# Kernel optimization log

Measured on AMD Instinct MI355X. Metric: run time of the kernel, lower is better.

The kernel has to match this reference:

```python
import jax, jax.numpy as jnp
import numpy as np
from jax import lax

B, C, L, O, H, W = 256, 768, 64, 768, 9, 9
C2, C3 = 2 * C // 3, C // 3  # convh_2 / convl_1 output channels


def _c1x1(x, w, b):
    # 1x1 conv, w: (out,in), x: (b,in,h,w)
    return jnp.einsum('oc,bchw->bohw', w, x) + b[None, :, None, None]


def _conv3x3(x, w, b=None):
    out = lax.conv_general_dilated(x, w, (1, 1), 'SAME', dimension_numbers=('NCHW', 'OIHW', 'NCHW'))
    if b is not None:
        out = out + b[None, :, None, None]
    return out


def _cossim(a, b):
    # torch F.cosine_similarity over dim=1, eps=1e-8
    num = jnp.sum(a * b, axis=1)
    den = jnp.maximum(jnp.linalg.norm(a, axis=1) * jnp.linalg.norm(b, axis=1), 1e-8)
    return num / den


def _ufilt1d(x, size, axis):
    # scipy.ndimage.uniform_filter1d, mode='reflect' (== numpy 'symmetric')
    r = size // 2
    pad = [(r, r) if a == axis else (0, 0) for a in range(x.ndim)]
    xp = jnp.moveaxis(jnp.pad(x, pad, mode='symmetric'), axis, -1)
    c = jnp.cumsum(xp, axis=-1)
    c = jnp.concatenate([jnp.zeros_like(c[..., :1]), c], axis=-1)
    out = (c[..., size:] - c[..., :-size]) / size
    return jnp.moveaxis(out, -1, axis)


def _ufilt(x, size):
    # skimage ssim with channel_axis=1 on a (b,c,h,w) array treats (b,h,w) as
    # the 3 spatial dims (batch included!) and loops over channels.
    for ax in (0, 2, 3):
        x = _ufilt1d(x, size, ax)
    return x


def _ssim_map(x, y, win=7):
    NP = win ** 3  # 3 spatial dims (b,h,w)
    cov_norm = NP / (NP - 1.0)
    c1, c2 = 0.01 ** 2, 0.03 ** 2  # data_range = 1.0
    ux, uy = _ufilt(x, win), _ufilt(y, win)
    vx = cov_norm * (_ufilt(x * x, win) - ux * ux)
    vy = cov_norm * (_ufilt(y * y, win) - uy * uy)
    vxy = cov_norm * (_ufilt(x * y, win) - ux * uy)
    return ((2 * ux * uy + c1) * (2 * vxy + c2)) / ((ux * ux + uy * uy + c1) * (vx + vy + c2))


def setup_inputs() -> dict:
    key = jax.random.key(0)
    ks = jax.random.split(key, 40)
    n = lambda i, shape, s=1.0: jax.random.normal(ks[i], shape, jnp.float32) * s
    return {
        'x': n(0, (B, C, H, W)),
        'y': n(1, (B, L, H, W)),
        'w_convh1': n(2, (C, C), C ** -0.5), 'b_convh1': n(3, (C,), 0.01),
        'w_conv1_1': n(4, (C, C), C ** -0.5), 'b_conv1_1': n(5, (C,), 0.01),
        'w_convh2': n(6, (C2, C), C ** -0.5), 'b_convh2': n(7, (C2,), 0.01),
        'w_convl1': n(8, (C3, L), L ** -0.5), 'b_convl1': n(9, (C3,), 0.01),
        'w_convh3': n(10, (1, C), C ** -0.5), 'b_convh3': n(11, (1,), 0.01),
        'w_convl2': n(12, (1, L), L ** -0.5), 'b_convl2': n(13, (1,), 0.01),
        'w_conv1_2': n(14, (2, 2), 0.7), 'b_conv1_2': n(15, (2,), 0.01),
        'w_convl3': n(16, (2, L), L ** -0.5), 'b_convl3': n(17, (2,), 0.01),
        'w_cc1': n(18, (1, 2), 0.7), 'b_cc1': n(19, (1,), 0.01),
        'w_pool': n(20, (2, 1, 3, 3), 1.0 / 3.0), 'b_pool': n(21, (2,), 0.01),
        'w_fc1': n(22, (324, 324), 324 ** -0.5), 'b_fc1': n(23, (324,), 0.01),
        'w_fc2': n(24, (81, 324), 324 ** -0.5), 'b_fc2': n(25, (81,), 0.01),
        'w_bconv': n(26, (O, C, 3, 3), (C * 9) ** -0.5),
        'bn_gamma': 1.0 + n(27, (O,), 0.1), 'bn_beta': n(28, (O,), 0.1),
        'bn_mean': n(29, (O,), 0.1),
        'bn_var': 1.0 + 0.1 * jax.random.uniform(ks[30], (O,), jnp.float32),
    }


def reference(x, y, w_convh1, b_convh1, w_conv1_1, b_conv1_1, w_convh2, b_convh2,
              w_convl1, b_convl1, w_convh3, b_convh3, w_convl2, b_convl2,
              w_conv1_2, b_conv1_2, w_convl3, b_convl3, w_cc1, b_cc1,
              w_pool, b_pool, w_fc1, b_fc1, w_fc2, b_fc2,
              w_bconv, bn_gamma, bn_beta, bn_mean, bn_var):
    b = x.shape[0]
    fuse_1 = _c1x1(x, w_convh1, b_convh1)                                   # (b,C,9,9)
    fuse_2 = _c1x1(jnp.concatenate([_c1x1(x, w_convh2, b_convh2),
                                    _c1x1(y, w_convl1, b_convl1)], axis=1),
                   w_conv1_1, b_conv1_1)                                     # (b,C,9,9)
    fuse_3 = _c1x1(jnp.concatenate([_c1x1(x, w_convh3, b_convh3),
                                    _c1x1(y, w_convl2, b_convl2)], axis=1),
                   w_conv1_2, b_conv1_2)                                     # (b,2,9,9)
    fuse_4 = _c1x1(y, w_convl3, b_convl3)                                    # (b,2,9,9)
    cor_1 = _cossim(fuse_1, fuse_2)[:, None]                                 # (b,1,9,9)
    ssim_value = lax.stop_gradient(_ssim_map(fuse_3, fuse_4))                # detach() in torch
    fuse2_1 = fuse_1 + 0.5 * (1.0 - cor_1) * fuse_2
    fuse2_2 = _c1x1(fuse_4 + ssim_value * fuse_3, w_cc1, b_cc1)              # (b,1,9,9)
    cor2_1 = _cossim(fuse2_1, jnp.broadcast_to(fuse2_2, fuse2_1.shape))[:, None]
    fuse3_1 = fuse2_1 + 0.5 * (1.0 - cor2_1 + _c1x1(ssim_value, w_cc1, b_cc1)) * fuse2_2
    # fuse2_2 has 1 channel -> channel mean == channel max == fuse2_2
    xc = jnp.concatenate([fuse2_2, _conv3x3(fuse2_2, w_pool, b_pool), fuse2_2], axis=1)  # (b,4,9,9)
    xc = xc.reshape(b, -1)
    h1 = jax.nn.gelu(xc @ w_fc1.T + b_fc1, approximate=False)
    xweight = jax.nn.leaky_relu(h1 @ w_fc2.T + b_fc2, 0.01).reshape(b, 1, H, W)
    xout = xweight * fuse3_1 + fuse3_1
    xout = _conv3x3(xout, w_bconv)
    scale = (bn_gamma / jnp.sqrt(bn_var + 1e-5))[None, :, None, None]
    xout = (xout - bn_mean[None, :, None, None]) * scale + bn_beta[None, :, None, None]
    return jax.nn.leaky_relu(xout, 0.01)
```

## Files before the change

kernel.cpp:

```cpp
#include <hip/hip_runtime.h>
#include <hip/hip_bf16.h>
#include <math.h>

#define BATCH 256
#define CCH 768
#define LCH 64
#define PP 81
#define CHW 3072

typedef __attribute__((ext_vector_type(8))) short short8v;
typedef __attribute__((ext_vector_type(4))) float f32x4;

#define GLL16(gp, lp) __builtin_amdgcn_global_load_lds( \
    (const __attribute__((address_space(1))) void*)(gp), \
    (__attribute__((address_space(3))) void*)(lp), 16, 0, 0)

__global__ __launch_bounds__(256) void kw_compose(
    const float* __restrict__ W11, const float* __restrict__ Wh2,
    const float* __restrict__ Wl1, const float* __restrict__ bh2,
    const float* __restrict__ bl1, const float* __restrict__ b11,
    const float* __restrict__ Wh1,
    __hip_bfloat16* __restrict__ WAp, __hip_bfloat16* __restrict__ WBp,
    __hip_bfloat16* __restrict__ Wh1p, float* __restrict__ beff)
{
    int o = blockIdx.x;
    int t = threadIdx.x;
    int ot = o >> 4, l15o = o & 15;
    const float* w11row = W11 + (size_t)o * CCH;
    for (int c = t; c < CCH; c += 256) {
        float s = 0.f;
        for (int k = 0; k < 512; ++k) s = fmaf(w11row[k], Wh2[(size_t)k*CCH + c], s);
        int ch = c >> 5, kg = (c >> 3) & 3, j = c & 7;
        size_t idx = (((size_t)ot*24 + ch) << 9) + (size_t)(kg*16 + l15o)*8 + j;
        WAp[idx]  = __float2bfloat16(s);
        Wh1p[idx] = __float2bfloat16(Wh1[(size_t)o*CCH + c]);
    }
    if (t < LCH) {
        float s = 0.f;
        for (int k = 0; k < 256; ++k) s = fmaf(w11row[512+k], Wl1[k*LCH + t], s);
        int ch = t >> 5, kg = (t >> 3) & 3, j = t & 7;
        size_t idx = (((size_t)ot*2 + ch) << 9) + (size_t)(kg*16 + l15o)*8 + j;
        WBp[idx] = __float2bfloat16(s);
    }
    if (t == 0) {
        float s = b11[o];
        for (int k = 0; k < 512; ++k) s = fmaf(w11row[k], bh2[k], s);
        for (int k = 0; k < 256; ++k) s = fmaf(w11row[512+k], bl1[k], s);
        beff[o] = s;
    }
}

__global__ __launch_bounds__(256) void k_wprep(
    const float* __restrict__ Wb, __hip_bfloat16* __restrict__ Wp)
{
    int ot = blockIdx.x;
    int i  = blockIdx.y*256 + threadIdx.x;
    int oi = i / 96, c8 = i - oi*96;
    const float* src = Wb + ((size_t)(ot*16 + oi)*CCH + c8*8)*9;
    int ch = c8 >> 2;
    int lane8 = (((c8 & 3)*16) + oi)*8;
    #pragma unroll
    for (int t = 0; t < 9; ++t) {
        short8v v;
        #pragma unroll
        for (int j = 0; j < 8; ++j) {
            __hip_bfloat16 h = __float2bfloat16(src[j*9 + t]);
            v[j] = __builtin_bit_cast(short, h);
        }
        *(short8v*)(Wp + ((((size_t)(t*48 + ot))*24 + ch) << 9) + lane8) = v;
    }
}

__global__ __launch_bounds__(256) void k_fcprep(
    const float* __restrict__ Wfc1, const float* __restrict__ Wfc2,
    float* __restrict__ T1, float* __restrict__ T2)
{
    int n = blockIdx.x*256 + threadIdx.x;
    if (n < 324*324) { int i = n / 324, j = n - i*324; T1[(size_t)j*324 + i] = Wfc1[n]; }
    if (n < 81*324)  { int q = n / 324, j = n - q*324; T2[(size_t)j*81 + q]  = Wfc2[n]; }
}

__global__ __launch_bounds__(256) void k_xprep_f34(
    const float* __restrict__ x, const float* __restrict__ y,
    const float* __restrict__ wh3, const float* __restrict__ bh3,
    const float* __restrict__ wl2, const float* __restrict__ bl2,
    const float* __restrict__ W12, const float* __restrict__ b12,
    const float* __restrict__ Wl3, const float* __restrict__ bl3,
    __hip_bfloat16* __restrict__ xT2, __hip_bfloat16* __restrict__ yT2,
    float* __restrict__ f3, float* __restrict__ f4, float* __restrict__ Af)
{
    int b = blockIdx.x;
    int tid = threadIdx.x;
    __shared__ float ls[64][82];
    __shared__ float red[243][4];
    __shared__ float zz[10][81];
    __shared__ float tb[10][81];
    int q = tid / 81, p81 = tid - q*81;
    bool act = tid < 243;
    for (int i = tid; i < 24*32; i += 256) {
        int ch = i >> 5, c = i & 31;
        xT2[(((size_t)b*24 + ch)*96 + 81)*32 + c] = __float2bfloat16(0.f);
    }
    if (tid < 2*32) {
        int ch = tid >> 5, c = tid & 31;
        yT2[(((size_t)b*2 + ch)*96 + 81)*32 + c] = __float2bfloat16(0.f);
    }
    float sx = 0.f;
    for (int c0 = 0; c0 < CCH; c0 += 64) {
        int ch0 = c0 >> 5;
        __syncthreads();
        for (int i = tid; i < 64*81; i += 256) {
            int c = i / 81, p = i - c*81;
            ls[c][p] = x[((size_t)b*CCH + c0 + c)*PP + p];
        }
        __syncthreads();
        for (int i = tid; i < 81*64; i += 256) {
            int p = i >> 6, c = i & 63;
            int ch = ch0 + (c >> 5), cc = c & 31;
            int s = cc >> 3, j = cc & 7;
            int slot = s ^ ((p >> 1) & 3);
            xT2[(((size_t)b*24 + ch)*96 + p)*32 + slot*8 + j] = __float2bfloat16(ls[c][p]);
        }
        if (act)
            for (int c = q; c < 64; c += 3)
                sx = fmaf(wh3[c0+c], ls[c][p81], sx);
    }
    __syncthreads();
    for (int i = tid; i < 64*81; i += 256) {
        int c = i / 81, p = i - c*81;
        ls[c][p] = y[((size_t)b*LCH + c)*PP + p];
    }
    __syncthreads();
    for (int i = tid; i < 81*64; i += 256) {
        int p = i >> 6, c = i & 63;
        int ch = c >> 5, cc = c & 31;
        int s = cc >> 3, j = cc & 7;
        int slot = s ^ ((p >> 1) & 3);
        yT2[(((size_t)b*2 + ch)*96 + p)*32 + slot*8 + j] = __float2bfloat16(ls[c][p]);
    }
    float sy = 0.f, s40 = 0.f, s41 = 0.f;
    if (act) {
        for (int c = q; c < 64; c += 3) {
            float v = ls[c][p81];
            sy  = fmaf(wl2[c], v, sy);
            s40 = fmaf(Wl3[c], v, s40);
            s41 = fmaf(Wl3[LCH+c], v, s41);
        }
        red[tid][0]=sx; red[tid][1]=sy; red[tid][2]=s40; red[tid][3]=s41;
    }
    __syncthreads();
    if (tid < 81) {
        float SX  = red[tid][0]+red[tid+81][0]+red[tid+162][0];
        float SY  = red[tid][1]+red[tid+81][1]+red[tid+162][1];
        float S40 = red[tid][2]+red[tid+81][2]+red[tid+162][2];
        float S41 = red[tid][3]+red[tid+81][3]+red[tid+162][3];
        float t3a = SX + bh3[0];
        float t3b = SY + bl2[0];
        float f30 = W12[0]*t3a + W12[1]*t3b + b12[0];
        float f31 = W12[2]*t3a + W12[3]*t3b + b12[1];
        float f40 = S40 + bl3[0];
        float f41 = S41 + bl3[1];
        f3[(b*2+0)*PP+tid] = f30; f3[(b*2+1)*PP+tid] = f31;
        f4[(b*2+0)*PP+tid] = f40; f4[(b*2+1)*PP+tid] = f41;
        zz[0][tid]=f30; zz[1][tid]=f40; zz[2][tid]=f30*f30; zz[3][tid]=f40*f40; zz[4][tid]=f30*f40;
        zz[5][tid]=f31; zz[6][tid]=f41; zz[7][tid]=f31*f31; zz[8][tid]=f41*f41; zz[9][tid]=f31*f41;
    }
    __syncthreads();
    for (int i = tid; i < 10*81; i += 256) {
        int f = i / 81, p = i - f*81;
        int yy = p/9, xx = p - yy*9;
        float s = 0.f;
        #pragma unroll
        for (int d = -3; d <= 3; ++d) {
            int j = xx + d;
            j = (j < 0) ? (-1-j) : ((j > 8) ? (17-j) : j);
            s += zz[f][yy*9+j];
        }
        tb[f][p] = s * (1.f/7.f);
    }
    __syncthreads();
    for (int i = tid; i < 10*81; i += 256) {
        int f = i / 81, p = i - f*81;
        int yy = p/9, xx = p - yy*9;
        float s = 0.f;
        #pragma unroll
        for (int d = -3; d <= 3; ++d) {
            int j = yy + d;
            j = (j < 0) ? (-1-j) : ((j > 8) ? (17-j) : j);
            s += tb[f][j*9+xx];
        }
        Af[((size_t)b*10 + f)*81 + p] = s * (1.f/7.f);
    }
}

__global__ __launch_bounds__(256) void k_ssim_b2(
    const float* __restrict__ A, float* __restrict__ U)
{
    int col0 = blockIdx.x * 32;
    int tid = threadIdx.x;
    __shared__ float lsb[256][33];
    for (int i = tid; i < 256*32; i += 256) {
        int j = i >> 5, cc = i & 31;
        int col = col0 + cc;
        lsb[j][cc] = (col < 810) ? A[(size_t)j*810 + col] : 0.f;
    }
    __syncthreads();
    for (int i = tid; i < 256*32; i += 256) {
        int b = i >> 5, cc = i & 31;
        float s = 0.f;
        #pragma unroll
        for (int d = -3; d <= 3; ++d) {
            int j = b + d;
            j = (j < 0) ? (-1-j) : ((j > 255) ? (511-j) : j);
            s += lsb[j][cc];
        }
        int col = col0 + cc;
        if (col < 810) U[(size_t)b*810 + col] = s * (1.f/7.f);
    }
}

__global__ __launch_bounds__(128) void k_fc(
    const float* __restrict__ U, const float* __restrict__ f3,
    const float* __restrict__ f4, const float* __restrict__ wcc,
    const float* __restrict__ bcc,
    const float* __restrict__ wpool, const float* __restrict__ bpool,
    const float* __restrict__ T1, const float* __restrict__ bfc1,
    const float* __restrict__ T2, const float* __restrict__ bfc2,
    float* __restrict__ f22, float* __restrict__ ccs,
    float* __restrict__ xw)
{
    int b = blockIdx.x;
    int tid = threadIdx.x;
    __shared__ float xc[324];
    __shared__ float h1[324];
    __shared__ float pr[2][81], ps[2][81];
    const float cov = 343.f/342.f, C1c = 1e-4f, C2c = 9e-4f;
    for (int i = tid; i < 162; i += 128) {
        int k = i / 81, p = i - k*81;
        const float* u = U + (size_t)b*810 + (k*5)*81 + p;
        float ux = u[0], uy = u[81], uxx = u[162], uyy = u[243], uxy = u[324];
        float vx = cov*(uxx - ux*ux), vy = cov*(uyy - uy*uy), vxy = cov*(uxy - ux*uy);
        float S = ((2.f*ux*uy + C1c)*(2.f*vxy + C2c)) /
                  ((ux*ux + uy*uy + C1c)*(vx + vy + C2c));
        float a = f4[(b*2+k)*81+p] + S*f3[(b*2+k)*81+p];
        pr[k][p] = wcc[k]*a;
        ps[k][p] = wcc[k]*S;
    }
    __syncthreads();
    if (tid < 81) {
        float fv = pr[0][tid] + pr[1][tid] + bcc[0];
        float cv = ps[0][tid] + ps[1][tid] + bcc[0];
        f22[b*81+tid] = fv;
        ccs[b*81+tid] = cv;
        xc[tid] = fv; xc[243+tid] = fv;
    }
    __syncthreads();
    for (int i = tid; i < 162; i += 128) {
        int k = i / 81, p = i - k*81;
        int yy = p/9, xx = p - yy*9;
        float s = bpool[k];
        #pragma unroll
        for (int dy = -1; dy <= 1; ++dy)
            #pragma unroll
            for (int dx = -1; dx <= 1; ++dx) {
                int Y = yy+dy, X = xx+dx;
                if (Y >= 0 && Y < 9 && X >= 0 && X < 9)
                    s = fmaf(wpool[k*9 + (dy+1)*3 + (dx+1)], xc[Y*9+X], s);
            }
        xc[81+i] = s;
    }
    __syncthreads();
    for (int i = tid; i < 324; i += 128) {
        float s = bfc1[i];
        for (int j = 0; j < 324; ++j) s = fmaf(T1[(size_t)j*324 + i], xc[j], s);
        h1[i] = 0.5f*s*(1.f + erff(s*0.70710678118654752f));
    }
    __syncthreads();
    for (int qq = tid; qq < 81; qq += 128) {
        float s = bfc2[qq];
        for (int j = 0; j < 324; ++j) s = fmaf(T2[(size_t)j*81 + qq], h1[j], s);
        xw[b*81+qq] = (s > 0.f) ? s : 0.01f*s;
    }
}

__global__ __launch_bounds__(256) void k_fuse12_mfma(
    const __hip_bfloat16* __restrict__ xT2,
    const __hip_bfloat16* __restrict__ yT2,
    const __hip_bfloat16* __restrict__ Wh1p,
    const __hip_bfloat16* __restrict__ WAp,
    const __hip_bfloat16* __restrict__ WBp,
    const float* __restrict__ bh1, const float* __restrict__ beff,
    __hip_bfloat16* __restrict__ f1, __hip_bfloat16* __restrict__ f2)
{
    int oy = blockIdx.x;
    int b  = blockIdx.y;
    int tid = threadIdx.x;
    int w    = tid >> 6;
    int g    = w >> 1;
    int nh   = w & 1;
    int lane = tid & 63;
    int l15  = lane & 15;
    int kg   = lane >> 4;

    int spoff[3];
    #pragma unroll
    for (int nl = 0; nl < 3; ++nl) {
        int p = (nh*3 + nl)*16 + l15;
        int sp = (p < PP) ? p : 81;
        spoff[nl] = sp*32 + ((kg ^ ((sp >> 1) & 3)) << 3);
    }

    f32x4 acc[6][3];
    #pragma unroll
    for (int m = 0; m < 6; ++m)
        #pragma unroll
        for (int nl = 0; nl < 3; ++nl)
            acc[m][nl] = (f32x4){0.f,0.f,0.f,0.f};

    const __hip_bfloat16* xb = xT2 + (size_t)b*24*CHW;
    const __hip_bfloat16* yb = yT2 + (size_t)b*2*CHW;
    const __hip_bfloat16* Wsel = g ? WAp : Wh1p;
    int otb = oy*6;

    for (int ch = 0; ch < 24; ++ch) {
        const __hip_bfloat16* cb = xb + (size_t)ch*CHW;
        short8v bf[3];
        #pragma unroll
        for (int nl = 0; nl < 3; ++nl)
            bf[nl] = *(const short8v*)&cb[spoff[nl]];
        short8v a[6];
        #pragma unroll
        for (int m = 0; m < 6; ++m)
            a[m] = *(const short8v*)(Wsel + ((((size_t)(otb + m))*24 + ch) << 9) + (lane<<3));
        #pragma unroll
        for (int nl = 0; nl < 3; ++nl)
            #pragma unroll
            for (int m = 0; m < 6; ++m)
                acc[m][nl] = __builtin_amdgcn_mfma_f32_16x16x32_bf16(a[m], bf[nl], acc[m][nl], 0, 0, 0);
    }

    if (g == 1) {
        for (int ch2 = 0; ch2 < 2; ++ch2) {
            const __hip_bfloat16* cb = yb + (size_t)ch2*CHW;
            short8v bf[3];
            #pragma unroll
            for (int nl = 0; nl < 3; ++nl)
                bf[nl] = *(const short8v*)&cb[spoff[nl]];
            short8v a[6];
            #pragma unroll
            for (int m = 0; m < 6; ++m)
                a[m] = *(const short8v*)(WBp + ((((size_t)(otb + m))*2 + ch2) << 9) + (lane<<3));
            #pragma unroll
            for (int nl = 0; nl < 3; ++nl)
                #pragma unroll
                for (int m = 0; m < 6; ++m)
                    acc[m][nl] = __builtin_amdgcn_mfma_f32_16x16x32_bf16(a[m], bf[nl], acc[m][nl], 0, 0, 0);
        }
    }

    __hip_bfloat16* dst = g ? f2 : f1;
    const float* bias = g ? beff : bh1;
    #pragma unroll
    for (int m = 0; m < 6; ++m) {
        #pragma unroll
        for (int r = 0; r < 4; ++r) {
            int o = (otb + m)*16 + kg*4 + r;
            float bb = bias[o];
            #pragma unroll
            for (int nl = 0; nl < 3; ++nl) {
                int p = (nh*3 + nl)*16 + l15;
                if (p < PP)
                    dst[((size_t)b*CCH + o)*PP + p] = __float2bfloat16(acc[m][nl][r] + bb);
            }
        }
    }
}

__global__ __launch_bounds__(256) void k_finalize(
    const __hip_bfloat16* __restrict__ f1, const __hip_bfloat16* __restrict__ f2,
    const float* __restrict__ f22, const float* __restrict__ ccs,
    const float* __restrict__ xw,
    __hip_bfloat16* __restrict__ inb2)
{
    int b = blockIdx.x;
    int tid = threadIdx.x;
    __shared__ float red[243][5];
    __shared__ float sal[81], sga[81], scm[81];
    __shared__ float ls[64][82];
    for (int i = tid; i < 24*32; i += 256) {
        int ch = i >> 5, c = i & 31;
        inb2[(((size_t)b*24 + ch)*96 + 81)*32 + c] = __float2bfloat16(0.f);
    }
    bool act = tid < 243;
    float Sxx=0.f, Syy=0.f, Sxy=0.f, Sx=0.f, Sy=0.f;
    const __hip_bfloat16* A = f1 + (size_t)b*CCH*PP;
    const __hip_bfloat16* C = f2 + (size_t)b*CCH*PP;
    if (act) {
        for (int c0 = 0; c0 < CCH; c0 += 3) {
            float u = __bfloat162float(A[(size_t)c0*PP + tid]);
            float v = __bfloat162float(C[(size_t)c0*PP + tid]);
            Sxx = fmaf(u,u,Sxx); Syy = fmaf(v,v,Syy); Sxy = fmaf(u,v,Sxy);
            Sx += u; Sy += v;
        }
        red[tid][0]=Sxx; red[tid][1]=Syy; red[tid][2]=Sxy; red[tid][3]=Sx; red[tid][4]=Sy;
    }
    __syncthreads();
    if (tid < 81) {
        float xx = red[tid][0]+red[tid+81][0]+red[tid+162][0];
        float yy = red[tid][1]+red[tid+81][1]+red[tid+162][1];
        float xy = red[tid][2]+red[tid+81][2]+red[tid+162][2];
        float sx = red[tid][3]+red[tid+81][3]+red[tid+162][3];
        float sy = red[tid][4]+red[tid+81][4]+red[tid+162][4];
        float cor1 = xy / fmaxf(sqrtf(xx)*sqrtf(yy), 1e-8f);
        float al = 0.5f*(1.f - cor1);
        float sum21 = sx + al*sy;
        float n21 = sqrtf(fmaxf(xx + 2.f*al*xy + al*al*yy, 0.f));
        int t = b*81 + tid;
        float fv = f22[t];
        float cor2 = (fv * sum21) / fmaxf(n21 * 27.712812921102035f * fabsf(fv), 1e-8f);
        float be = 0.5f*(1.f - cor2 + ccs[t]);
        sal[tid] = al;
        sga[tid] = be * fv;
        scm[tid] = 1.f + xw[t];
    }
    for (int c0 = 0; c0 < CCH; c0 += 64) {
        int ch0 = c0 >> 5;
        __syncthreads();
        for (int i = tid; i < 64*81; i += 256) {
            int c = i / 81, p = i - c*81;
            size_t gidx = ((size_t)b*CCH + c0 + c)*PP + p;
            float u = __bfloat162float(f1[gidx]);
            float v = __bfloat162float(f2[gidx]);
            ls[c][p] = scm[p]*(u + sal[p]*v + sga[p]);
        }
        __syncthreads();
        for (int i = tid; i < 81*64; i += 256) {
            int p = i >> 6, c = i & 63;
            int ch = ch0 + (c >> 5), cc = c & 31;
            int s = cc >> 3, j = cc & 7;
            int slot = s ^ ((p >> 1) & 3);
            inb2[(((size_t)b*24 + ch)*96 + p)*32 + slot*8 + j] = __float2bfloat16(ls[c][p]);
        }
    }
}

__global__ __launch_bounds__(256, 2) void k_bconv_mfma(
    const __hip_bfloat16* __restrict__ inb2,
    const __hip_bfloat16* __restrict__ Wp,
    const float* __restrict__ bn_g, const float* __restrict__ bn_b,
    const float* __restrict__ bn_m, const float* __restrict__ bn_v,
    float* __restrict__ out)
{
    int oy = blockIdx.x;
    int b0 = blockIdx.y * 2;
    int tid = threadIdx.x;
    int w    = tid >> 6;
    int bi   = w >> 1;
    int nh   = w & 1;
    int lane = tid & 63;
    int l15  = lane & 15;
    int kg   = lane >> 4;

    __shared__ __align__(16) __hip_bfloat16 ls[6*CHW];

    int spoff[9][3];
    #pragma unroll
    for (int t = 0; t < 9; ++t) {
        int dy = t/3 - 1, dx = t%3 - 1;
        #pragma unroll
        for (int nl = 0; nl < 3; ++nl) {
            int p = (nh*3 + nl)*16 + l15;
            int yy = p/9, xx = p - yy*9;
            int Y = yy + dy, X = xx + dx;
            bool ok = (p < PP) && (Y >= 0) && (Y < 9) && (X >= 0) && (X < 9);
            int sp = ok ? (Y*9 + X) : 81;
            spoff[t][nl] = sp*32 + ((kg ^ ((sp >> 1) & 3)) << 3);
        }
    }

    f32x4 acc[6][3];
    #pragma unroll
    for (int m = 0; m < 6; ++m)
        #pragma unroll
        for (int nl = 0; nl < 3; ++nl)
            acc[m][nl] = (f32x4){0.f,0.f,0.f,0.f};

    const __hip_bfloat16* img0 = inb2 + (size_t)(b0    )*24*CHW;
    const __hip_bfloat16* img1 = inb2 + (size_t)(b0 + 1)*24*CHW;
    int otb = oy*6;

    for (int grp = 0; grp < 8; ++grp) {
        __syncthreads();
        #pragma unroll
        for (int k = 0; k < 9; ++k) {
            int it = w + 4*k;
            int bb = it / 18;
            int r  = it - bb*18;
            int cc = r / 6, sub = r - cc*6;
            const __hip_bfloat16* src =
                (bb ? img1 : img0) + (size_t)(grp*3 + cc)*CHW + sub*512;
            GLL16(src + lane*8, &ls[(size_t)(bb*3 + cc)*CHW + sub*512]);
        }
        __syncthreads();
        for (int cc = 0; cc < 3; ++cc) {
            int ch = grp*3 + cc;
            const __hip_bfloat16* lb = &ls[(size_t)(bi*3 + cc)*CHW];
            #pragma unroll
            for (int t = 0; t < 9; ++t) {
                short8v a[6];
                #pragma unroll
                for (int m = 0; m < 6; ++m)
                    a[m] = *(const short8v*)(Wp + (((size_t)(t*48 + otb + m)*24 + ch) << 9) + (lane<<3));
                #pragma unroll
                for (int nl = 0; nl < 3; ++nl) {
                    short8v bf = *(const short8v*)&lb[spoff[t][nl]];
                    #pragma unroll
                    for (int m = 0; m < 6; ++m)
                        acc[m][nl] = __builtin_amdgcn_mfma_f32_16x16x32_bf16(a[m], bf, acc[m][nl], 0, 0, 0);
                }
            }
        }
    }

    int b = b0 + bi;
    #pragma unroll
    for (int m = 0; m < 6; ++m) {
        #pragma unroll
        for (int r = 0; r < 4; ++r) {
            int o = (otb + m)*16 + kg*4 + r;
            float sc = bn_g[o] * rsqrtf(bn_v[o] + 1e-5f);
            float mn = bn_m[o], bt = bn_b[o];
            #pragma unroll
            for (int nl = 0; nl < 3; ++nl) {
                int p = (nh*3 + nl)*16 + l15;
                if (p < PP) {
                    float v = (acc[m][nl][r] - mn) * sc + bt;
                    out[((size_t)b*CCH + o)*PP + p] = (v > 0.f) ? v : 0.01f*v;
                }
            }
        }
    }
}

extern "C" void kernel_launch(void* const* d_in, const int* in_sizes, int n_in,
                              void* d_out, int out_size, void* d_ws, size_t ws_size,
                              hipStream_t stream)
{
    (void)in_sizes; (void)n_in; (void)out_size; (void)ws_size;
    const float* x    = (const float*)d_in[0];
    const float* y    = (const float*)d_in[1];
    const float* Wh1  = (const float*)d_in[2];
    const float* bh1  = (const float*)d_in[3];
    const float* W11  = (const float*)d_in[4];
    const float* b11  = (const float*)d_in[5];
    const float* Wh2  = (const float*)d_in[6];
    const float* bh2  = (const float*)d_in[7];
    const float* Wl1  = (const float*)d_in[8];
    const float* bl1  = (const float*)d_in[9];
    const float* wh3  = (const float*)d_in[10];
    const float* bh3  = (const float*)d_in[11];
    const float* wl2  = (const float*)d_in[12];
    const float* bl2  = (const float*)d_in[13];
    const float* W12  = (const float*)d_in[14];
    const float* b12  = (const float*)d_in[15];
    const float* Wl3  = (const float*)d_in[16];
    const float* bl3  = (const float*)d_in[17];
    const float* wcc  = (const float*)d_in[18];
    const float* bcc  = (const float*)d_in[19];
    const float* wpool= (const float*)d_in[20];
    const float* bpool= (const float*)d_in[21];
    const float* Wfc1 = (const float*)d_in[22];
    const float* bfc1 = (const float*)d_in[23];
    const float* Wfc2 = (const float*)d_in[24];
    const float* bfc2 = (const float*)d_in[25];
    const float* Wb   = (const float*)d_in[26];
    const float* bng  = (const float*)d_in[27];
    const float* bnb  = (const float*)d_in[28];
    const float* bnm  = (const float*)d_in[29];
    const float* bnv  = (const float*)d_in[30];
    float* out = (float*)d_out;
    float* ws = (float*)d_ws;

    size_t off = 0;
    float* beff  = ws + off; off += CCH;
    float* f3    = ws + off; off += BATCH*2*PP;
    float* f4    = ws + off; off += BATCH*2*PP;
    float* Af    = ws + off; off += BATCH*10*PP;
    float* Uf    = ws + off; off += BATCH*10*PP;
    float* f22   = ws + off; off += BATCH*PP;
    float* ccs   = ws + off; off += BATCH*PP;
    float* xw    = ws + off; off += BATCH*PP;
    float* T1    = ws + off; off += 324*324;
    float* T2    = ws + off; off += 324*81;
    off = (off + 3) & ~(size_t)3;
    __hip_bfloat16* Wh1p = (__hip_bfloat16*)(ws + off); off += (size_t)48*24*512/2;
    __hip_bfloat16* WAp  = (__hip_bfloat16*)(ws + off); off += (size_t)48*24*512/2;
    __hip_bfloat16* WBp  = (__hip_bfloat16*)(ws + off); off += (size_t)48*2*512/2;
    __hip_bfloat16* yT2  = (__hip_bfloat16*)(ws + off); off += (size_t)BATCH*2*CHW/2;
    __hip_bfloat16* f1b  = (__hip_bfloat16*)(ws + off); off += (size_t)BATCH*CCH*PP/2;
    __hip_bfloat16* f2b  = (__hip_bfloat16*)(ws + off); off += (size_t)BATCH*CCH*PP/2;
    off = (off + 3) & ~(size_t)3;
    __hip_bfloat16* inb2 = (__hip_bfloat16*)(ws + off); off += (size_t)BATCH*24*CHW/2;
    __hip_bfloat16* Wp   = (__hip_bfloat16*)(ws + off); off += (size_t)9*48*24*512/2;
    __hip_bfloat16* xT2 = inb2;

    kw_compose<<<dim3(CCH), dim3(256), 0, stream>>>(W11, Wh2, Wl1, bh2, bl1, b11, Wh1, WAp, WBp, Wh1p, beff);
    k_wprep<<<dim3(48, 6), dim3(256), 0, stream>>>(Wb, Wp);
    k_fcprep<<<dim3(411), dim3(256), 0, stream>>>(Wfc1, Wfc2, T1, T2);
    k_xprep_f34<<<dim3(BATCH), dim3(256), 0, stream>>>(x, y, wh3, bh3, wl2, bl2, W12, b12, Wl3, bl3, xT2, yT2, f3, f4, Af);
    k_ssim_b2<<<dim3(26), dim3(256), 0, stream>>>(Af, Uf);
    k_fc<<<dim3(BATCH), dim3(128), 0, stream>>>(Uf, f3, f4, wcc, bcc, wpool, bpool, T1, bfc1, T2, bfc2, f22, ccs, xw);
    k_fuse12_mfma<<<dim3(8, BATCH), dim3(256), 0, stream>>>(xT2, yT2, Wh1p, WAp, WBp, bh1, beff, f1b, f2b);
    k_finalize<<<dim3(BATCH), dim3(256), 0, stream>>>(f1b, f2b, f22, ccs, xw, inb2);
    k_bconv_mfma<<<dim3(8, BATCH/2), dim3(256), 0, stream>>>(inb2, Wp, bng, bnb, bnm, bnv, out);
}
```

Measured before the change: 695.0 us.

## Merge weight-prep kernels and read conv inputs directly from global in bconv

Three weight-preparation kernels (weight composition, 3x3 conv weight packing, fc transposes) become one kernel that branches on block index, saving two launches. The 3x3 conv MFMA kernel drops its shared-memory staging via global_load_lds and its barriers. Each 128-thread block now handles a single image, and the B fragments are read straight from global/L2 with the 3 spatial loads hoisted before the MFMAs. This trades LDS staging and sync overhead for more uncached-pattern global reads and twice as many blocks.

```diff
diff --git a/kernel.cpp b/kernel.cpp
--- a/kernel.cpp
+++ b/kernel.cpp
@@ -11,73 +11,67 @@
 typedef __attribute__((ext_vector_type(8))) short short8v;
 typedef __attribute__((ext_vector_type(4))) float f32x4;
 
-#define GLL16(gp, lp) __builtin_amdgcn_global_load_lds( \
-    (const __attribute__((address_space(1))) void*)(gp), \
-    (__attribute__((address_space(3))) void*)(lp), 16, 0, 0)
-
-__global__ __launch_bounds__(256) void kw_compose(
+__global__ __launch_bounds__(256) void k_prep(
     const float* __restrict__ W11, const float* __restrict__ Wh2,
     const float* __restrict__ Wl1, const float* __restrict__ bh2,
     const float* __restrict__ bl1, const float* __restrict__ b11,
-    const float* __restrict__ Wh1,
+    const float* __restrict__ Wh1, const float* __restrict__ Wb,
+    const float* __restrict__ Wfc1, const float* __restrict__ Wfc2,
     __hip_bfloat16* __restrict__ WAp, __hip_bfloat16* __restrict__ WBp,
-    __hip_bfloat16* __restrict__ Wh1p, float* __restrict__ beff)
-{
-    int o = blockIdx.x;
+    __hip_bfloat16* __restrict__ Wh1p, float* __restrict__ beff,
+    __hip_bfloat16* __restrict__ Wp,
+    float* __restrict__ T1, float* __restrict__ T2)
+{
+    int blk = blockIdx.x;
     int t = threadIdx.x;
-    int ot = o >> 4, l15o = o & 15;
-    const float* w11row = W11 + (size_t)o * CCH;
-    for (int c = t; c < CCH; c += 256) {
-        float s = 0.f;
-        for (int k = 0; k < 512; ++k) s = fmaf(w11row[k], Wh2[(size_t)k*CCH + c], s);
-        int ch = c >> 5, kg = (c >> 3) & 3, j = c & 7;
-        size_t idx = (((size_t)ot*24 + ch) << 9) + (size_t)(kg*16 + l15o)*8 + j;
-        WAp[idx]  = __float2bfloat16(s);
-        Wh1p[idx] = __float2bfloat16(Wh1[(size_t)o*CCH + c]);
-    }
-    if (t < LCH) {
-        float s = 0.f;
-        for (int k = 0; k < 256; ++k) s = fmaf(w11row[512+k], Wl1[k*LCH + t], s);
-        int ch = t >> 5, kg = (t >> 3) & 3, j = t & 7;
-        size_t idx = (((size_t)ot*2 + ch) << 9) + (size_t)(kg*16 + l15o)*8 + j;
-        WBp[idx] = __float2bfloat16(s);
-    }
-    if (t == 0) {
-        float s = b11[o];
-        for (int k = 0; k < 512; ++k) s = fmaf(w11row[k], bh2[k], s);
-        for (int k = 0; k < 256; ++k) s = fmaf(w11row[512+k], bl1[k], s);
-        beff[o] = s;
-    }
-}
-
-__global__ __launch_bounds__(256) void k_wprep(
-    const float* __restrict__ Wb, __hip_bfloat16* __restrict__ Wp)
-{
-    int ot = blockIdx.x;
-    int i  = blockIdx.y*256 + threadIdx.x;
-    int oi = i / 96, c8 = i - oi*96;
-    const float* src = Wb + ((size_t)(ot*16 + oi)*CCH + c8*8)*9;
-    int ch = c8 >> 2;
-    int lane8 = (((c8 & 3)*16) + oi)*8;
-    #pragma unroll
-    for (int t = 0; t < 9; ++t) {
-        short8v v;
-        #pragma unroll
-        for (int j = 0; j < 8; ++j) {
-            __hip_bfloat16 h = __float2bfloat16(src[j*9 + t]);
-            v[j] = __builtin_bit_cast(short, h);
-        }
-        *(short8v*)(Wp + ((((size_t)(t*48 + ot))*24 + ch) << 9) + lane8) = v;
-    }
-}
-
-__global__ __launch_bounds__(256) void k_fcprep(
-    const float* __restrict__ Wfc1, const float* __restrict__ Wfc2,
-    float* __restrict__ T1, float* __restrict__ T2)
-{
-    int n = blockIdx.x*256 + threadIdx.x;
-    if (n < 324*324) { int i = n / 324, j = n - i*324; T1[(size_t)j*324 + i] = Wfc1[n]; }
-    if (n < 81*324)  { int q = n / 324, j = n - q*324; T2[(size_t)j*81 + q]  = Wfc2[n]; }
+    if (blk < CCH) {
+        int o = blk;
+        int ot = o >> 4, l15o = o & 15;
+        const float* w11row = W11 + (size_t)o * CCH;
+        for (int c = t; c < CCH; c += 256) {
+            float s = 0.f;
+            for (int k = 0; k < 512; ++k) s = fmaf(w11row[k], Wh2[(size_t)k*CCH + c], s);
+            int ch = c >> 5, kg = (c >> 3) & 3, j = c & 7;
+            size_t idx = (((size_t)ot*24 + ch) << 9) + (size_t)(kg*16 + l15o)*8 + j;
+            WAp[idx]  = __float2bfloat16(s);
+            Wh1p[idx] = __float2bfloat16(Wh1[(size_t)o*CCH + c]);
+        }
+        if (t < LCH) {
+            float s = 0.f;
+            for (int k = 0; k < 256; ++k) s = fmaf(w11row[512+k], Wl1[k*LCH + t], s);
+            int ch = t >> 5, kg = (t >> 3) & 3, j = t & 7;
+            size_t idx = (((size_t)ot*2 + ch) << 9) + (size_t)(kg*16 + l15o)*8 + j;
+            WBp[idx] = __float2bfloat16(s);
+        }
+        if (t == 0) {
+            float s = b11[o];
+            for (int k = 0; k < 512; ++k) s = fmaf(w11row[k], bh2[k], s);
+            for (int k = 0; k < 256; ++k) s = fmaf(w11row[512+k], bl1[k], s);
+            beff[o] = s;
+        }
+    } else if (blk < CCH + 288) {
+        int id = blk - CCH;
+        int ot = id / 6;
+        int i  = (id - ot*6)*256 + t;
+        int oi = i / 96, c8 = i - oi*96;
+        const float* src = Wb + ((size_t)(ot*16 + oi)*CCH + c8*8)*9;
+        int ch = c8 >> 2;
+        int lane8 = (((c8 & 3)*16) + oi)*8;
+        #pragma unroll
+        for (int tt = 0; tt < 9; ++tt) {
+            short8v v;
+            #pragma unroll
+            for (int j = 0; j < 8; ++j) {
+                __hip_bfloat16 h = __float2bfloat16(src[j*9 + tt]);
+                v[j] = __builtin_bit_cast(short, h);
+            }
+            *(short8v*)(Wp + ((((size_t)(tt*48 + ot))*24 + ch) << 9) + lane8) = v;
+        }
+    } else {
+        int n = (blk - CCH - 288)*256 + t;
+        if (n < 324*324) { int i = n / 324, j = n - i*324; T1[(size_t)j*324 + i] = Wfc1[n]; }
+        if (n < 81*324)  { int q = n / 324, j = n - q*324; T2[(size_t)j*81 + q]  = Wfc2[n]; }
+    }
 }
 
 __global__ __launch_bounds__(256) void k_xprep_f34(
@@ -444,7 +438,7 @@
     }
 }
 
-__global__ __launch_bounds__(256, 2) void k_bconv_mfma(
+__global__ __launch_bounds__(128) void k_bconv_mfma(
     const __hip_bfloat16* __restrict__ inb2,
     const __hip_bfloat16* __restrict__ Wp,
     const float* __restrict__ bn_g, const float* __restrict__ bn_b,
@@ -452,16 +446,12 @@
     float* __restrict__ out)
 {
     int oy = blockIdx.x;
-    int b0 = blockIdx.y * 2;
+    int b  = blockIdx.y;
     int tid = threadIdx.x;
     int w    = tid >> 6;
-    int bi   = w >> 1;
-    int nh   = w & 1;
     int lane = tid & 63;
     int l15  = lane & 15;
     int kg   = lane >> 4;
-
-    __shared__ __align__(16) __hip_bfloat16 ls[6*CHW];
 
     int spoff[9][3];
     #pragma unroll
@@ -469,7 +459,7 @@
         int dy = t/3 - 1, dx = t%3 - 1;
         #pragma unroll
         for (int nl = 0; nl < 3; ++nl) {
-            int p = (nh*3 + nl)*16 + l15;
+            int p = (w*3 + nl)*16 + l15;
             int yy = p/9, xx = p - yy*9;
             int Y = yy + dy, X = xx + dx;
             bool ok = (p < PP) && (Y >= 0) && (Y < 9) && (X >= 0) && (X < 9);
@@ -485,44 +475,29 @@
         for (int nl = 0; nl < 3; ++nl)
             acc[m][nl] = (f32x4){0.f,0.f,0.f,0.f};
 
-    const __hip_bfloat16* img0 = inb2 + (size_t)(b0    )*24*CHW;
-    const __hip_bfloat16* img1 = inb2 + (size_t)(b0 + 1)*24*CHW;
+    const __hip_bfloat16* img = inb2 + (size_t)b*24*CHW;
     int otb = oy*6;
 
-    for (int grp = 0; grp < 8; ++grp) {
-        __syncthreads();
-        #pragma unroll
-        for (int k = 0; k < 9; ++k) {
-            int it = w + 4*k;
-            int bb = it / 18;
-            int r  = it - bb*18;
-            int cc = r / 6, sub = r - cc*6;
-            const __hip_bfloat16* src =
-                (bb ? img1 : img0) + (size_t)(grp*3 + cc)*CHW + sub*512;
-            GLL16(src + lane*8, &ls[(size_t)(bb*3 + cc)*CHW + sub*512]);
-        }
-        __syncthreads();
-        for (int cc = 0; cc < 3; ++cc) {
-            int ch = grp*3 + cc;
-            const __hip_bfloat16* lb = &ls[(size_t)(bi*3 + cc)*CHW];
-            #pragma unroll
-            for (int t = 0; t < 9; ++t) {
-                short8v a[6];
+    for (int ch = 0; ch < 24; ++ch) {
+        const __hip_bfloat16* cb = img + (size_t)ch*CHW;
+        #pragma unroll
+        for (int t = 0; t < 9; ++t) {
+            short8v bf[3];
+            #pragma unroll
+            for (int nl = 0; nl < 3; ++nl)
+                bf[nl] = *(const short8v*)&cb[spoff[t][nl]];
+            short8v a[6];
+            #pragma unroll
+            for (int m = 0; m < 6; ++m)
+                a[m] = *(const short8v*)(Wp + (((size_t)(t*48 + otb + m)*24 + ch) << 9) + (lane<<3));
+            #pragma unroll
+            for (int nl = 0; nl < 3; ++nl)
                 #pragma unroll
                 for (int m = 0; m < 6; ++m)
-                    a[m] = *(const short8v*)(Wp + (((size_t)(t*48 + otb + m)*24 + ch) << 9) + (lane<<3));
-                #pragma unroll
-                for (int nl = 0; nl < 3; ++nl) {
-                    short8v bf = *(const short8v*)&lb[spoff[t][nl]];
-                    #pragma unroll
-                    for (int m = 0; m < 6; ++m)
-                        acc[m][nl] = __builtin_amdgcn_mfma_f32_16x16x32_bf16(a[m], bf, acc[m][nl], 0, 0, 0);
-                }
-            }
-        }
-    }
-
-    int b = b0 + bi;
+                    acc[m][nl] = __builtin_amdgcn_mfma_f32_16x16x32_bf16(a[m], bf[nl], acc[m][nl], 0, 0, 0);
+        }
+    }
+
     #pragma unroll
     for (int m = 0; m < 6; ++m) {
         #pragma unroll
@@ -532,7 +507,7 @@
             float mn = bn_m[o], bt = bn_b[o];
             #pragma unroll
             for (int nl = 0; nl < 3; ++nl) {
-                int p = (nh*3 + nl)*16 + l15;
+                int p = (w*3 + nl)*16 + l15;
                 if (p < PP) {
                     float v = (acc[m][nl][r] - mn) * sc + bt;
                     out[((size_t)b*CCH + o)*PP + p] = (v > 0.f) ? v : 0.01f*v;
@@ -604,13 +579,13 @@
     __hip_bfloat16* Wp   = (__hip_bfloat16*)(ws + off); off += (size_t)9*48*24*512/2;
     __hip_bfloat16* xT2 = inb2;
 
-    kw_compose<<<dim3(CCH), dim3(256), 0, stream>>>(W11, Wh2, Wl1, bh2, bl1, b11, Wh1, WAp, WBp, Wh1p, beff);
-    k_wprep<<<dim3(48, 6), dim3(256), 0, stream>>>(Wb, Wp);
-    k_fcprep<<<dim3(411), dim3(256), 0, stream>>>(Wfc1, Wfc2, T1, T2);
+    k_prep<<<dim3(CCH + 288 + 411), dim3(256), 0, stream>>>(
+        W11, Wh2, Wl1, bh2, bl1, b11, Wh1, Wb, Wfc1, Wfc2,
+        WAp, WBp, Wh1p, beff, Wp, T1, T2);
     k_xprep_f34<<<dim3(BATCH), dim3(256), 0, stream>>>(x, y, wh3, bh3, wl2, bl2, W12, b12, Wl3, bl3, xT2, yT2, f3, f4, Af);
     k_ssim_b2<<<dim3(26), dim3(256), 0, stream>>>(Af, Uf);
     k_fc<<<dim3(BATCH), dim3(128), 0, stream>>>(Uf, f3, f4, wcc, bcc, wpool, bpool, T1, bfc1, T2, bfc2, f22, ccs, xw);
     k_fuse12_mfma<<<dim3(8, BATCH), dim3(256), 0, stream>>>(xT2, yT2, Wh1p, WAp, WBp, bh1, beff, f1b, f2b);
     k_finalize<<<dim3(BATCH), dim3(256), 0, stream>>>(f1b, f2b, f22, ccs, xw, inb2);
-    k_bconv_mfma<<<dim3(8, BATCH/2), dim3(256), 0, stream>>>(inb2, Wp, bng, bnb, bnm, bnv, out);
-}
+    k_bconv_mfma<<<dim3(8, BATCH), dim3(128), 0, stream>>>(inb2, Wp, bng, bnb, bnm, bnv, out);
+}
```

New measurement: 909.3 us. 1.31x slower.
